# Kernel tuning notes

Measured on AMD Instinct MI355X. Metric: run time of the kernel, lower is better.

The kernel has to match this reference:

```python
import jax, jax.numpy as jnp
import numpy as np

B, T, D, H, E = 32, 512, 768, 12, 6  # batch, seq(=input_size), n_embd, num_heads, per-head dim
DFF = 4 * D
EPS = 1e-5


def setup_inputs() -> dict:
    key = jax.random.key(0)
    ks = jax.random.split(key, 10)
    s = 0.02
    return {
        "x": jax.random.normal(ks[0], (B, T, D), jnp.float32),
        "Wq": jax.random.normal(ks[1], (H, D, E), jnp.float32) * s,
        "Wk": jax.random.normal(ks[2], (H, D, E), jnp.float32) * s,
        "Wv": jax.random.normal(ks[3], (H, D, E), jnp.float32) * s,
        "Wo": jax.random.normal(ks[4], (H * E, D), jnp.float32) * s,
        "bo": jnp.zeros((D,), jnp.float32),
        "W1": jax.random.normal(ks[5], (D, DFF), jnp.float32) * s,
        "b1": jnp.zeros((DFF,), jnp.float32),
        "W2": jax.random.normal(ks[6], (DFF, D), jnp.float32) * s,
        "b2": jnp.zeros((D,), jnp.float32),
        "g1": jnp.ones((D,), jnp.float32),
        "beta1": jnp.zeros((D,), jnp.float32),
        "g2": jnp.ones((D,), jnp.float32),
        "beta2": jnp.zeros((D,), jnp.float32),
    }


def _layernorm(x, g, b):
    m = jnp.mean(x, axis=-1, keepdims=True)
    v = jnp.var(x, axis=-1, keepdims=True)  # biased, matches torch LayerNorm
    return (x - m) * jax.lax.rsqrt(v + EPS) * g + b


def reference(x, Wq, Wk, Wv, Wo, bo, W1, b1, W2, b2, g1, beta1, g2, beta2):
    # --- pre-LN multi-head causal attention (dropout = identity, eval mode) ---
    xn = _layernorm(x, g1, beta1)
    q = jnp.einsum("btd,hde->bhte", xn, Wq)
    k = jnp.einsum("btd,hde->bhte", xn, Wk)
    v = jnp.einsum("btd,hde->bhte", xn, Wv)
    scores = jnp.einsum("bhte,bhse->bhts", q, k) * (E ** -0.5)
    causal = jnp.tril(jnp.ones((T, T), dtype=bool))
    scores = jnp.where(causal, scores, -jnp.inf)
    w = jax.nn.softmax(scores, axis=-1)
    o = jnp.einsum("bhts,bhse->bhte", w, v)
    o = o.transpose(0, 2, 1, 3).reshape(B, T, H * E)  # concat heads -> [B,T,72]
    x = x + o @ Wo + bo
    # --- pre-LN feed-forward ---
    y = _layernorm(x, g2, beta2)
    ff = jax.nn.relu(y @ W1 + b1) @ W2 + b2
    return x + ff
```

## Files before the change

### kernel.cpp

```cpp
#include <hip/hip_runtime.h>
#include <hip/hip_bf16.h>

#define BT 16384
#define DIM 768
#define NH 12
#define DFF 3072

typedef __attribute__((ext_vector_type(8))) short short8;
typedef __attribute__((ext_vector_type(4))) float floatx4;
typedef __attribute__((ext_vector_type(4))) unsigned short ushort4b;

using bf16 = __hip_bfloat16;

static __device__ __forceinline__ float b2f(bf16 v) { return __bfloat162float(v); }
static __device__ __forceinline__ bf16 f2b(float v) { return __float2bfloat16(v); }

static __device__ __forceinline__ void gload_lds16(const void* g, void* l) {
    __builtin_amdgcn_global_load_lds(
        (const __attribute__((address_space(1))) unsigned int*)g,
        (__attribute__((address_space(3))) unsigned int*)l, 16, 0, 0);
}

__global__ __launch_bounds__(256) void pack_small_kernel(
    const float* __restrict__ Wq, const float* __restrict__ Wk, const float* __restrict__ Wv,
    const float* __restrict__ Wo, bf16* __restrict__ wqkv, bf16* __restrict__ wo_t)
{
    int i = blockIdx.x * 256 + threadIdx.x;
    const int S0 = 256 * 768, S1 = 768 * 96;
    if (i < S0) {
        int c = i / 768, dd = i % 768;
        float v = 0.f;
        if (c < 216) {
            int sel = c / 72, cc = c % 72, h = cc / 6, e = cc % 6;
            const float* W = (sel == 0) ? Wq : (sel == 1) ? Wk : Wv;
            v = W[((size_t)h * 768 + dd) * 6 + e];
        }
        wqkv[i] = f2b(v);
    } else if ((i -= S0) < S1) {
        int n = i / 96, r = i % 96;
        wo_t[i] = f2b(r < 72 ? Wo[r * 768 + n] : 0.f);
    }
}

__global__ __launch_bounds__(256) void transpose_kernel(
    const float* __restrict__ in, bf16* __restrict__ out, int R, int C)
{
    __shared__ float t[32][33];
    int c0 = blockIdx.x * 32, r0 = blockIdx.y * 32;
    int cx = threadIdx.x & 31, ry = threadIdx.x >> 5;
#pragma unroll
    for (int j = 0; j < 4; j++)
        t[ry + j * 8][cx] = in[(size_t)(r0 + ry + j * 8) * C + c0 + cx];
    __syncthreads();
    int rx = cx, cy = ry;
#pragma unroll
    for (int j = 0; j < 4; j++)
        out[(size_t)(c0 + cy + j * 8) * R + r0 + rx] = f2b(t[rx][cy + j * 8]);
}

__global__ __launch_bounds__(192) void ln_kernel(
    const float* __restrict__ x, const float* __restrict__ g, const float* __restrict__ be,
    bf16* __restrict__ out)
{
    int row = blockIdx.x;
    int tid = threadIdx.x;
    const float4* xr = (const float4*)(x + (size_t)row * DIM);
    float4 v = xr[tid];
    float s = v.x + v.y + v.z + v.w;
    float s2 = v.x * v.x + v.y * v.y + v.z * v.z + v.w * v.w;
#pragma unroll
    for (int off = 32; off; off >>= 1) {
        s += __shfl_down(s, off);
        s2 += __shfl_down(s2, off);
    }
    __shared__ float red[6];
    int wv = tid >> 6, ln = tid & 63;
    if (ln == 0) { red[wv] = s; red[3 + wv] = s2; }
    __syncthreads();
    float ts = red[0] + red[1] + red[2];
    float ts2 = red[3] + red[4] + red[5];
    float mean = ts * (1.f / 768.f);
    float var = ts2 * (1.f / 768.f) - mean * mean;
    float rstd = rsqrtf(var + 1e-5f);
    int c = tid * 4;
    float o0 = (v.x - mean) * rstd * g[c + 0] + be[c + 0];
    float o1 = (v.y - mean) * rstd * g[c + 1] + be[c + 1];
    float o2 = (v.z - mean) * rstd * g[c + 2] + be[c + 2];
    float o3 = (v.w - mean) * rstd * g[c + 3] + be[c + 3];
    bf16 h0 = f2b(o0), h1 = f2b(o1), h2 = f2b(o2), h3 = f2b(o3);
    ushort4b pk;
    pk[0] = *(unsigned short*)&h0; pk[1] = *(unsigned short*)&h1;
    pk[2] = *(unsigned short*)&h2; pk[3] = *(unsigned short*)&h3;
    *(ushort4b*)(out + (size_t)row * DIM + c) = pk;
}

template <int N, int K, int NSLAB, bool RELU, bool BIAS, bool RES, bool BF16OUT>
__global__ __launch_bounds__(256) void gemm_kernel(
    const bf16* __restrict__ A, const bf16* __restrict__ Bt,
    const float* __restrict__ bias, const float* __restrict__ res,
    void* __restrict__ Cv, int M)
{
    constexpr int STAGE = NSLAB * 2 * 128 * 32 * 2;
    constexpr int SMEM_BYTES = BF16OUT ? (STAGE > 128 * 136 * 2 ? STAGE : 128 * 136 * 2) : STAGE;
    __shared__ __align__(16) char smem[SMEM_BYTES];
    bf16* lA = (bf16*)smem;
    bf16* lB = lA + NSLAB * 128 * 32;

    const int tid = threadIdx.x;
    const int bm = blockIdx.x * 128;
    const int bn = blockIdx.y * 128;
    const int wave = tid >> 6, lane = tid & 63;
    const int wm = (wave >> 1) * 64, wn = (wave & 1) * 64;
    const int quad = lane >> 4, l16 = lane & 15;
    const int lrow = lane >> 2;
    const int lkc = (lane & 3) * 8;

    floatx4 acc[4][4] = {};

    for (int k0 = 0; k0 < K; k0 += NSLAB * 32) {
#pragma unroll
        for (int s = 0; s < NSLAB; s++) {
#pragma unroll
            for (int it = 0; it < 2; it++) {
                int r = wave * 32 + it * 16;
                gload_lds16(A + (size_t)(bm + r + lrow) * K + k0 + s * 32 + lkc,
                            lA + s * 4096 + r * 32);
                gload_lds16(Bt + (size_t)(bn + r + lrow) * K + k0 + s * 32 + lkc,
                            lB + s * 4096 + r * 32);
            }
        }
        __syncthreads();
#pragma unroll
        for (int s = 0; s < NSLAB; s++) {
            short8 af[4], bfr[4];
#pragma unroll
            for (int mt = 0; mt < 4; mt++)
                af[mt] = *(const short8*)(lA + s * 4096 + (wm + mt * 16 + l16) * 32 + quad * 8);
#pragma unroll
            for (int nt = 0; nt < 4; nt++)
                bfr[nt] = *(const short8*)(lB + s * 4096 + (wn + nt * 16 + l16) * 32 + quad * 8);
#pragma unroll
            for (int mt = 0; mt < 4; mt++)
#pragma unroll
                for (int nt = 0; nt < 4; nt++)
                    acc[mt][nt] = __builtin_amdgcn_mfma_f32_16x16x32_bf16(af[mt], bfr[nt], acc[mt][nt], 0, 0, 0);
        }
        __syncthreads();
    }

    if constexpr (BF16OUT) {
        bf16* ltile = (bf16*)smem;
#pragma unroll
        for (int mt = 0; mt < 4; mt++) {
#pragma unroll
            for (int nt = 0; nt < 4; nt++) {
                int tc = wn + nt * 16 + l16;
#pragma unroll
                for (int r = 0; r < 4; r++) {
                    int tr = wm + mt * 16 + quad * 4 + r;
                    float v0 = acc[mt][nt][r];
                    if constexpr (BIAS) v0 += bias[bn + tc];
                    if constexpr (RELU) v0 = fmaxf(v0, 0.f);
                    ltile[tr * 136 + tc] = f2b(v0);
                }
            }
        }
        __syncthreads();
        bf16* C = (bf16*)Cv;
        int rr0 = tid >> 4, col8 = (tid & 15) * 8;
        int gc = bn + col8;
#pragma unroll
        for (int p = 0; p < 8; p++) {
            int rr = p * 16 + rr0;
            if (gc < N)
                *(short8*)(C + (size_t)(bm + rr) * N + gc) =
                    *(const short8*)(ltile + rr * 136 + col8);
        }
    } else {
        float* C = (float*)Cv;
#pragma unroll
        for (int mt = 0; mt < 4; mt++) {
#pragma unroll
            for (int nt = 0; nt < 4; nt++) {
                int gc = bn + wn + nt * 16 + l16;
                if (gc < N) {
#pragma unroll
                    for (int r = 0; r < 4; r++) {
                        int gr = bm + wm + mt * 16 + quad * 4 + r;
                        float v0 = acc[mt][nt][r];
                        if constexpr (BIAS) v0 += bias[gc];
                        if constexpr (RES) v0 += res[(size_t)gr * N + gc];
                        if constexpr (RELU) v0 = fmaxf(v0, 0.f);
                        C[(size_t)gr * N + gc] = v0;
                    }
                }
            }
        }
    }
}

template <int N, int K, bool RELU, bool BIAS, bool RES, bool BF16OUT>
__global__ __launch_bounds__(256, 2) void gemm256_kernel(
    const bf16* __restrict__ A, const bf16* __restrict__ Bt,
    const float* __restrict__ bias, const float* __restrict__ res,
    void* __restrict__ Cv, int M)
{
    __shared__ __align__(16) char smem[49152];
    bf16* lA = (bf16*)smem;
    bf16* lB = lA + 2 * 256 * 32;

    const int tid = threadIdx.x;
    const int bm = blockIdx.x * 256;
    const int bn = blockIdx.y * 128;
    const int wave = tid >> 6, lane = tid & 63;
    const int quad = lane >> 4, l16 = lane & 15;
    const int lrow = lane >> 2;
    const int lkc = (lane & 3) * 8;

    floatx4 acc[4][8] = {};

    for (int k0 = 0; k0 < K; k0 += 64) {
#pragma unroll
        for (int s = 0; s < 2; s++) {
#pragma unroll
            for (int it = 0; it < 4; it++) {
                int r = (wave * 4 + it) * 16;
                gload_lds16(A + (size_t)(bm + r + lrow) * K + k0 + s * 32 + lkc,
                            lA + s * 8192 + r * 32);
            }
#pragma unroll
            for (int it = 0; it < 2; it++) {
                int r = (wave * 2 + it) * 16;
                gload_lds16(Bt + (size_t)(bn + r + lrow) * K + k0 + s * 32 + lkc,
                            lB + s * 4096 + r * 32);
            }
        }
        __syncthreads();
#pragma unroll
        for (int s = 0; s < 2; s++) {
            short8 af[4], bfr[8];
#pragma unroll
            for (int mt = 0; mt < 4; mt++)
                af[mt] = *(const short8*)(lA + s * 8192 + (wave * 64 + mt * 16 + l16) * 32 + quad * 8);
#pragma unroll
            for (int nt = 0; nt < 8; nt++)
                bfr[nt] = *(const short8*)(lB + s * 4096 + (nt * 16 + l16) * 32 + quad * 8);
#pragma unroll
            for (int mt = 0; mt < 4; mt++)
#pragma unroll
                for (int nt = 0; nt < 8; nt++)
                    acc[mt][nt] = __builtin_amdgcn_mfma_f32_16x16x32_bf16(af[mt], bfr[nt], acc[mt][nt], 0, 0, 0);
        }
        __syncthreads();
    }

    float bv[8];
    if constexpr (BIAS) {
#pragma unroll
        for (int nt = 0; nt < 8; nt++) bv[nt] = bias[bn + nt * 16 + l16];
    }
#pragma unroll
    for (int p = 0; p < 4; p++) {
        if (wave == p) {
            if constexpr (BF16OUT) {
                bf16* tile = (bf16*)smem;
#pragma unroll
                for (int mt = 0; mt < 4; mt++)
#pragma unroll
                    for (int nt = 0; nt < 8; nt++)
#pragma unroll
                        for (int r = 0; r < 4; r++) {
                            float v0 = acc[mt][nt][r];
                            if constexpr (BIAS) v0 += bv[nt];
                            if constexpr (RELU) v0 = fmaxf(v0, 0.f);
                            tile[(mt * 16 + quad * 4 + r) * 136 + nt * 16 + l16] = f2b(v0);
                        }
            } else {
                float* tile = (float*)smem;
#pragma unroll
                for (int mt = 0; mt < 4; mt++)
#pragma unroll
                    for (int nt = 0; nt < 8; nt++)
#pragma unroll
                        for (int r = 0; r < 4; r++) {
                            float v0 = acc[mt][nt][r];
                            if constexpr (BIAS) v0 += bv[nt];
                            if constexpr (RELU) v0 = fmaxf(v0, 0.f);
                            tile[(mt * 16 + quad * 4 + r) * 132 + nt * 16 + l16] = v0;
                        }
            }
        }
        __syncthreads();
        if constexpr (BF16OUT) {
            const bf16* tile = (const bf16*)smem;
            bf16* C = (bf16*)Cv;
            int col8 = (tid & 15) * 8, r0 = tid >> 4;
#pragma unroll
            for (int j = 0; j < 4; j++) {
                int rr = j * 16 + r0;
                *(short8*)(C + (size_t)(bm + p * 64 + rr) * N + bn + col8) =
                    *(const short8*)(tile + rr * 136 + col8);
            }
        } else {
            const float* tile = (const float*)smem;
            float* C = (float*)Cv;
            int col4 = (tid & 31) * 4, r0 = tid >> 5;
#pragma unroll
            for (int j = 0; j < 8; j++) {
                int rr = j * 8 + r0;
                float4 v = *(const float4*)(tile + rr * 132 + col4);
                size_t gi = (size_t)(bm + p * 64 + rr) * N + bn + col4;
                if constexpr (RES) {
                    float4 rv = *(const float4*)(res + gi);
                    v.x += rv.x; v.y += rv.y; v.z += rv.z; v.w += rv.w;
                }
                *(float4*)(C + gi) = v;
            }
        }
        __syncthreads();
    }
}

__global__ __launch_bounds__(256) void attn_kernel(const bf16* __restrict__ qkv, bf16* __restrict__ o_pad)
{
    int blk = blockIdx.x;
    int half = blk & 1;
    int bh = blk >> 1;
    int b = bh / NH, h = bh % NH;
    int wave = threadIdx.x >> 6, lane = threadIdx.x & 63;
    const int jmap0[4] = {0, 2, 5, 7}, jmap1[4] = {1, 3, 4, 6};
    int j = half ? jmap1[wave] : jmap0[wave];
    int t = j * 64 + lane;
    int smax = half ? 448 : 512;

    __shared__ float ks[512 * 6];
    __shared__ float vs[512 * 6];
    const bf16* base = qkv + (size_t)b * 512 * 216;
    for (int i = threadIdx.x; i < smax * 6; i += 256) {
        int s = i / 6, e = i % 6;
        ks[i] = b2f(base[s * 216 + 72 + h * 6 + e]);
        vs[i] = b2f(base[s * 216 + 144 + h * 6 + e]);
    }
    __syncthreads();

    float q0 = b2f(base[t * 216 + h * 6 + 0]);
    float q1 = b2f(base[t * 216 + h * 6 + 1]);
    float q2 = b2f(base[t * 216 + h * 6 + 2]);
    float q3 = b2f(base[t * 216 + h * 6 + 3]);
    float q4 = b2f(base[t * 216 + h * 6 + 4]);
    float q5 = b2f(base[t * 216 + h * 6 + 5]);

    const float scale = 0.4082482904638630f;
    float m = -1e30f, l = 0.f;
    float o0 = 0, o1 = 0, o2 = 0, o3 = 0, o4 = 0, o5 = 0;
    for (int s = 0; s <= t; s++) {
        const float* kk = &ks[s * 6];
        float sc = (q0 * kk[0] + q1 * kk[1] + q2 * kk[2] + q3 * kk[3] + q4 * kk[4] + q5 * kk[5]) * scale;
        float nm = fmaxf(m, sc);
        float alpha = __expf(m - nm);
        float p = __expf(sc - nm);
        l = l * alpha + p;
        const float* vv = &vs[s * 6];
        o0 = o0 * alpha + p * vv[0];
        o1 = o1 * alpha + p * vv[1];
        o2 = o2 * alpha + p * vv[2];
        o3 = o3 * alpha + p * vv[3];
        o4 = o4 * alpha + p * vv[4];
        o5 = o5 * alpha + p * vv[5];
        m = nm;
    }
    float inv = 1.f / l;
    bf16* orow = o_pad + (size_t)(b * 512 + t) * 96 + h * 6;
    orow[0] = f2b(o0 * inv);
    orow[1] = f2b(o1 * inv);
    orow[2] = f2b(o2 * inv);
    orow[3] = f2b(o3 * inv);
    orow[4] = f2b(o4 * inv);
    orow[5] = f2b(o5 * inv);
}

extern "C" void kernel_launch(void* const* d_in, const int* in_sizes, int n_in,
                              void* d_out, int out_size, void* d_ws, size_t ws_size,
                              hipStream_t stream)
{
    const float* x   = (const float*)d_in[0];
    const float* Wq  = (const float*)d_in[1];
    const float* Wk  = (const float*)d_in[2];
    const float* Wv  = (const float*)d_in[3];
    const float* Wo  = (const float*)d_in[4];
    const float* bo  = (const float*)d_in[5];
    const float* W1  = (const float*)d_in[6];
    const float* b1  = (const float*)d_in[7];
    const float* W2  = (const float*)d_in[8];
    const float* b2  = (const float*)d_in[9];
    const float* g1  = (const float*)d_in[10];
    const float* be1 = (const float*)d_in[11];
    const float* g2  = (const float*)d_in[12];
    const float* be2 = (const float*)d_in[13];

    char* ws = (char*)d_ws;
    size_t off = 0;
    auto alloc = [&](size_t bytes) {
        void* p = ws + off;
        off = (off + bytes + 255) & ~(size_t)255;
        return p;
    };
    bf16*  xn    = (bf16*)alloc((size_t)BT * DIM * 2);
    bf16*  qkvb  = (bf16*)alloc((size_t)BT * 216 * 2);
    bf16*  o_pad = (bf16*)alloc((size_t)BT * 96 * 2);
    float* x1    = (float*)alloc((size_t)BT * DIM * 4);
    bf16*  ffb   = (bf16*)alloc((size_t)BT * DFF * 2);
    bf16*  wqkv  = (bf16*)alloc((size_t)256 * 768 * 2);
    bf16*  wo_t  = (bf16*)alloc((size_t)768 * 96 * 2);
    bf16*  w1t   = (bf16*)alloc((size_t)3072 * 768 * 2);
    bf16*  w2t   = (bf16*)alloc((size_t)768 * 3072 * 2);

    const int PACK_N = 256 * 768 + 768 * 96;
    pack_small_kernel<<<(PACK_N + 255) / 256, 256, 0, stream>>>(Wq, Wk, Wv, Wo, wqkv, wo_t);
    transpose_kernel<<<dim3(3072 / 32, 768 / 32), 256, 0, stream>>>(W1, w1t, 768, 3072);
    transpose_kernel<<<dim3(768 / 32, 3072 / 32), 256, 0, stream>>>(W2, w2t, 3072, 768);

    ln_kernel<<<BT, 192, 0, stream>>>(x, g1, be1, xn);
    gemm_kernel<216, 768, 2, false, false, false, true><<<dim3(128, 2), 256, 0, stream>>>(
        xn, wqkv, nullptr, nullptr, qkvb, BT);
    attn_kernel<<<32 * NH * 2, 256, 0, stream>>>(qkvb, o_pad);
    gemm_kernel<768, 96, 1, false, true, true, false><<<dim3(128, 6), 256, 0, stream>>>(
        o_pad, wo_t, bo, x, x1, BT);
    ln_kernel<<<BT, 192, 0, stream>>>(x1, g2, be2, xn);
    gemm256_kernel<3072, 768, true, true, false, true><<<dim3(64, 24), 256, 0, stream>>>(
        xn, w1t, b1, nullptr, ffb, BT);
    gemm256_kernel<768, 3072, false, true, true, false><<<dim3(64, 6), 256, 0, stream>>>(
        ffb, w2t, b2, x1, (float*)d_out, BT);
}
```

Measured before the change: 461.9 us.

## Use warp-specialized producer/consumer double-buffered GEMM for QKV and FFN layers

Replaces the 256x128 FFN GEMM and the QKV GEMM with a 512-thread kernel. Four producer waves stage the next 64-wide K slice into a second LDS buffer with global_load_lds while four consumer waves run MFMA on the current one. The aim is to overlap global-to-LDS loads with compute instead of serializing load, barrier and compute in each iteration. In exchange, the tile shrinks to 128x128, so there is less reuse per block, half the waves do no math, and each block uses 64KB of LDS, which may limit occupancy.

```diff
diff --git a/kernel.cpp b/kernel.cpp
--- a/kernel.cpp
+++ b/kernel.cpp
@@ -94,6 +94,136 @@
     *(ushort4b*)(out + (size_t)row * DIM + c) = pk;
 }
 
+template <int N, int K, bool RELU, bool BIAS, bool RES, bool BF16OUT>
+__global__ __launch_bounds__(512, 4) void gemm_pc_kernel(
+    const bf16* __restrict__ A, const bf16* __restrict__ Bt,
+    const float* __restrict__ bias, const float* __restrict__ res,
+    void* __restrict__ Cv, int M)
+{
+    __shared__ __align__(16) char smem[65536];
+    bf16* lA = (bf16*)smem;
+    bf16* lB = (bf16*)(smem + 32768);
+
+    const int tid = threadIdx.x;
+    const int bm = blockIdx.x * 128, bn = blockIdx.y * 128;
+    const int wave = tid >> 6, lane = tid & 63;
+    const bool producer = wave < 4;
+    const int lrow = lane >> 2, lkc = (lane & 3) * 8;
+    const int quad = lane >> 4, l16 = lane & 15;
+    const int cw = wave - 4;
+    const int wm = (cw >> 1) * 64, wn = (cw & 1) * 64;
+
+    constexpr int NIT = K / 64;
+    floatx4 acc[4][4] = {};
+    float bv[4];
+    if (BIAS && !producer) {
+#pragma unroll
+        for (int nt = 0; nt < 4; nt++) bv[nt] = bias[bn + wn + nt * 16 + l16];
+    }
+
+    auto stage = [&](int buf, int k0) {
+#pragma unroll
+        for (int s = 0; s < 2; s++)
+#pragma unroll
+            for (int it = 0; it < 2; it++) {
+                int r = (wave * 2 + it) * 16;
+                gload_lds16(A + (size_t)(bm + r + lrow) * K + k0 + s * 32 + lkc,
+                            lA + buf * 8192 + s * 4096 + r * 32);
+                gload_lds16(Bt + (size_t)(bn + r + lrow) * K + k0 + s * 32 + lkc,
+                            lB + buf * 8192 + s * 4096 + r * 32);
+            }
+    };
+
+    if (producer) stage(0, 0);
+    __syncthreads();
+
+    for (int i = 0; i < NIT; i++) {
+        int buf = i & 1;
+        if (producer) {
+            if (i + 1 < NIT) stage(buf ^ 1, (i + 1) * 64);
+        } else {
+#pragma unroll
+            for (int s = 0; s < 2; s++) {
+                short8 af[4], bfr[4];
+#pragma unroll
+                for (int mt = 0; mt < 4; mt++)
+                    af[mt] = *(const short8*)(lA + buf * 8192 + s * 4096 + (wm + mt * 16 + l16) * 32 + quad * 8);
+#pragma unroll
+                for (int nt = 0; nt < 4; nt++)
+                    bfr[nt] = *(const short8*)(lB + buf * 8192 + s * 4096 + (wn + nt * 16 + l16) * 32 + quad * 8);
+#pragma unroll
+                for (int mt = 0; mt < 4; mt++)
+#pragma unroll
+                    for (int nt = 0; nt < 4; nt++)
+                        acc[mt][nt] = __builtin_amdgcn_mfma_f32_16x16x32_bf16(af[mt], bfr[nt], acc[mt][nt], 0, 0, 0);
+            }
+        }
+        __syncthreads();
+    }
+
+    if constexpr (BF16OUT) {
+        bf16* ltile = (bf16*)smem;
+        if (!producer) {
+#pragma unroll
+            for (int mt = 0; mt < 4; mt++)
+#pragma unroll
+                for (int nt = 0; nt < 4; nt++)
+#pragma unroll
+                    for (int r = 0; r < 4; r++) {
+                        float v0 = acc[mt][nt][r];
+                        if constexpr (BIAS) v0 += bv[nt];
+                        if constexpr (RELU) v0 = fmaxf(v0, 0.f);
+                        ltile[(wm + mt * 16 + quad * 4 + r) * 136 + wn + nt * 16 + l16] = f2b(v0);
+                    }
+        }
+        __syncthreads();
+        bf16* C = (bf16*)Cv;
+        int rr0 = tid >> 4;
+        int col8 = (tid & 15) * 8;
+        int gc = bn + col8;
+#pragma unroll
+        for (int p = 0; p < 4; p++) {
+            int rr = p * 32 + rr0;
+            if (gc < N)
+                *(short8*)(C + (size_t)(bm + rr) * N + gc) =
+                    *(const short8*)(ltile + rr * 136 + col8);
+        }
+    } else {
+        float* ltile = (float*)smem;
+        float* C = (float*)Cv;
+#pragma unroll
+        for (int p = 0; p < 2; p++) {
+            if (!producer && (wm >> 6) == p) {
+#pragma unroll
+                for (int mt = 0; mt < 4; mt++)
+#pragma unroll
+                    for (int nt = 0; nt < 4; nt++)
+#pragma unroll
+                        for (int r = 0; r < 4; r++) {
+                            float v0 = acc[mt][nt][r];
+                            if constexpr (BIAS) v0 += bv[nt];
+                            if constexpr (RELU) v0 = fmaxf(v0, 0.f);
+                            ltile[(mt * 16 + quad * 4 + r) * 132 + wn + nt * 16 + l16] = v0;
+                        }
+            }
+            __syncthreads();
+            int col4 = (tid & 31) * 4, r0 = tid >> 5;
+#pragma unroll
+            for (int j = 0; j < 4; j++) {
+                int rr = j * 16 + r0;
+                float4 v = *(const float4*)(ltile + rr * 132 + col4);
+                size_t gi = (size_t)(bm + p * 64 + rr) * N + bn + col4;
+                if constexpr (RES) {
+                    float4 rv = *(const float4*)(res + gi);
+                    v.x += rv.x; v.y += rv.y; v.z += rv.z; v.w += rv.w;
+                }
+                *(float4*)(C + gi) = v;
+            }
+            __syncthreads();
+        }
+    }
+}
+
 template <int N, int K, int NSLAB, bool RELU, bool BIAS, bool RES, bool BF16OUT>
 __global__ __launch_bounds__(256) void gemm_kernel(
     const bf16* __restrict__ A, const bf16* __restrict__ Bt,
@@ -196,128 +326,6 @@
                 }
             }
         }
-    }
-}
-
-template <int N, int K, bool RELU, bool BIAS, bool RES, bool BF16OUT>
-__global__ __launch_bounds__(256, 2) void gemm256_kernel(
-    const bf16* __restrict__ A, const bf16* __restrict__ Bt,
-    const float* __restrict__ bias, const float* __restrict__ res,
-    void* __restrict__ Cv, int M)
-{
-    __shared__ __align__(16) char smem[49152];
-    bf16* lA = (bf16*)smem;
-    bf16* lB = lA + 2 * 256 * 32;
-
-    const int tid = threadIdx.x;
-    const int bm = blockIdx.x * 256;
-    const int bn = blockIdx.y * 128;
-    const int wave = tid >> 6, lane = tid & 63;
-    const int quad = lane >> 4, l16 = lane & 15;
-    const int lrow = lane >> 2;
-    const int lkc = (lane & 3) * 8;
-
-    floatx4 acc[4][8] = {};
-
-    for (int k0 = 0; k0 < K; k0 += 64) {
-#pragma unroll
-        for (int s = 0; s < 2; s++) {
-#pragma unroll
-            for (int it = 0; it < 4; it++) {
-                int r = (wave * 4 + it) * 16;
-                gload_lds16(A + (size_t)(bm + r + lrow) * K + k0 + s * 32 + lkc,
-                            lA + s * 8192 + r * 32);
-            }
-#pragma unroll
-            for (int it = 0; it < 2; it++) {
-                int r = (wave * 2 + it) * 16;
-                gload_lds16(Bt + (size_t)(bn + r + lrow) * K + k0 + s * 32 + lkc,
-                            lB + s * 4096 + r * 32);
-            }
-        }
-        __syncthreads();
-#pragma unroll
-        for (int s = 0; s < 2; s++) {
-            short8 af[4], bfr[8];
-#pragma unroll
-            for (int mt = 0; mt < 4; mt++)
-                af[mt] = *(const short8*)(lA + s * 8192 + (wave * 64 + mt * 16 + l16) * 32 + quad * 8);
-#pragma unroll
-            for (int nt = 0; nt < 8; nt++)
-                bfr[nt] = *(const short8*)(lB + s * 4096 + (nt * 16 + l16) * 32 + quad * 8);
-#pragma unroll
-            for (int mt = 0; mt < 4; mt++)
-#pragma unroll
-                for (int nt = 0; nt < 8; nt++)
-                    acc[mt][nt] = __builtin_amdgcn_mfma_f32_16x16x32_bf16(af[mt], bfr[nt], acc[mt][nt], 0, 0, 0);
-        }
-        __syncthreads();
-    }
-
-    float bv[8];
-    if constexpr (BIAS) {
-#pragma unroll
-        for (int nt = 0; nt < 8; nt++) bv[nt] = bias[bn + nt * 16 + l16];
-    }
-#pragma unroll
-    for (int p = 0; p < 4; p++) {
-        if (wave == p) {
-            if constexpr (BF16OUT) {
-                bf16* tile = (bf16*)smem;
-#pragma unroll
-                for (int mt = 0; mt < 4; mt++)
-#pragma unroll
-                    for (int nt = 0; nt < 8; nt++)
-#pragma unroll
-                        for (int r = 0; r < 4; r++) {
-                            float v0 = acc[mt][nt][r];
-                            if constexpr (BIAS) v0 += bv[nt];
-                            if constexpr (RELU) v0 = fmaxf(v0, 0.f);
-                            tile[(mt * 16 + quad * 4 + r) * 136 + nt * 16 + l16] = f2b(v0);
-                        }
-            } else {
-                float* tile = (float*)smem;
-#pragma unroll
-                for (int mt = 0; mt < 4; mt++)
-#pragma unroll
-                    for (int nt = 0; nt < 8; nt++)
-#pragma unroll
-                        for (int r = 0; r < 4; r++) {
-                            float v0 = acc[mt][nt][r];
-                            if constexpr (BIAS) v0 += bv[nt];
-                            if constexpr (RELU) v0 = fmaxf(v0, 0.f);
-                            tile[(mt * 16 + quad * 4 + r) * 132 + nt * 16 + l16] = v0;
-                        }
-            }
-        }
-        __syncthreads();
-        if constexpr (BF16OUT) {
-            const bf16* tile = (const bf16*)smem;
-            bf16* C = (bf16*)Cv;
-            int col8 = (tid & 15) * 8, r0 = tid >> 4;
-#pragma unroll
-            for (int j = 0; j < 4; j++) {
-                int rr = j * 16 + r0;
-                *(short8*)(C + (size_t)(bm + p * 64 + rr) * N + bn + col8) =
-                    *(const short8*)(tile + rr * 136 + col8);
-            }
-        } else {
-            const float* tile = (const float*)smem;
-            float* C = (float*)Cv;
-            int col4 = (tid & 31) * 4, r0 = tid >> 5;
-#pragma unroll
-            for (int j = 0; j < 8; j++) {
-                int rr = j * 8 + r0;
-                float4 v = *(const float4*)(tile + rr * 132 + col4);
-                size_t gi = (size_t)(bm + p * 64 + rr) * N + bn + col4;
-                if constexpr (RES) {
-                    float4 rv = *(const float4*)(res + gi);
-                    v.x += rv.x; v.y += rv.y; v.z += rv.z; v.w += rv.w;
-                }
-                *(float4*)(C + gi) = v;
-            }
-        }
-        __syncthreads();
     }
 }
 
@@ -421,14 +429,14 @@
     transpose_kernel<<<dim3(768 / 32, 3072 / 32), 256, 0, stream>>>(W2, w2t, 3072, 768);
 
     ln_kernel<<<BT, 192, 0, stream>>>(x, g1, be1, xn);
-    gemm_kernel<216, 768, 2, false, false, false, true><<<dim3(128, 2), 256, 0, stream>>>(
+    gemm_pc_kernel<216, 768, false, false, false, true><<<dim3(128, 2), 512, 0, stream>>>(
         xn, wqkv, nullptr, nullptr, qkvb, BT);
     attn_kernel<<<32 * NH * 2, 256, 0, stream>>>(qkvb, o_pad);
     gemm_kernel<768, 96, 1, false, true, true, false><<<dim3(128, 6), 256, 0, stream>>>(
         o_pad, wo_t, bo, x, x1, BT);
     ln_kernel<<<BT, 192, 0, stream>>>(x1, g2, be2, xn);
-    gemm256_kernel<3072, 768, true, true, false, true><<<dim3(64, 24), 256, 0, stream>>>(
+    gemm_pc_kernel<3072, 768, true, true, false, true><<<dim3(128, 24), 512, 0, stream>>>(
         xn, w1t, b1, nullptr, ffb, BT);
-    gemm256_kernel<768, 3072, false, true, true, false><<<dim3(64, 6), 256, 0, stream>>>(
+    gemm_pc_kernel<768, 3072, false, true, true, false><<<dim3(128, 6), 512, 0, stream>>>(
         ffb, w2t, b2, x1, (float*)d_out, BT);
 }
```

Result: slower. 474.6 us (+2.7%).
